# Performance work log

Hardware: AMD Instinct MI355X
Metric: run time of the kernel (lower is better)

The kernel has to match this reference:

```python
import jax, jax.numpy as jnp
import numpy as np

EPS = 1e-6
ALPHA = 0.2  # LeakyReLU negative slope


def layer_norm(x, g, b):
    mu = jnp.mean(x, axis=-1, keepdims=True)
    var = jnp.mean(jnp.square(x - mu), axis=-1, keepdims=True)
    return (x - mu) * jax.lax.rsqrt(var + EPS) * g + b


def graph_attention(x, bias, W, a_src, a_dst):
    # x: [B,N,D], bias: [B,N,N], W: [D, H*Dh], a_src/a_dst: [H, Dh]
    B, N, D = x.shape
    H, Dh = a_src.shape
    h = jnp.einsum('bnd,dhk->bhnk', x, W.reshape(D, H, Dh))  # [B,H,N,Dh]
    s = jnp.einsum('bhnk,hk->bhn', h, a_src)                 # source term
    t = jnp.einsum('bhnk,hk->bhn', h, a_dst)                 # target term
    e = jax.nn.leaky_relu(s[:, :, :, None] + t[:, :, None, :], ALPHA)
    e = e + bias[:, None, :, :]                              # graph mask/bias
    attn = jax.nn.softmax(e, axis=-1)                        # [B,H,N,N]
    out = jnp.einsum('bhij,bhjk->bhik', attn, h)             # [B,H,N,Dh]
    return out.transpose(0, 2, 1, 3).reshape(B, N, H * Dh)


def setup_inputs() -> dict:
    key = jax.random.key(0)
    ks = jax.random.split(key, 8)
    B, N, D, H = 2, 2048, 512, 8
    Dh = D // H
    sc = 1.0 / np.sqrt(D)
    return {
        'x': jax.random.normal(ks[0], (B, N, D), jnp.float32),
        'bias': jax.random.normal(ks[1], (B, N, N), jnp.float32),
        'W1': jax.random.normal(ks[2], (D, D), jnp.float32) * sc,
        'a_src1': jax.random.normal(ks[3], (H, Dh), jnp.float32) * sc,
        'a_dst1': jax.random.normal(ks[4], (H, Dh), jnp.float32) * sc,
        'g1': jnp.ones((D,), jnp.float32),
        'b1': jnp.zeros((D,), jnp.float32),
        'W2': jax.random.normal(ks[5], (D, D), jnp.float32) * sc,
        'a_src2': jax.random.normal(ks[6], (1, D), jnp.float32) * sc,
        'a_dst2': jax.random.normal(ks[7], (1, D), jnp.float32) * sc,
        'g2': jnp.ones((D,), jnp.float32),
        'b2': jnp.zeros((D,), jnp.float32),
    }


def reference(x, bias, W1, a_src1, a_dst1, g1, b1, W2, a_src2, a_dst2, g2, b2):
    # dropout is identity in eval mode
    attn_in = layer_norm(x, g1, b1)
    attn = graph_attention(attn_in, bias, W1, a_src1, a_dst1) + x
    attn_in2 = layer_norm(attn, g2, b2)
    out = graph_attention(attn_in2, bias, W2, a_src2, a_dst2) + attn
    return out
```

## Files before the change

kernel.cpp:

```cpp
#include <hip/hip_runtime.h>
#include <math.h>

#define NB 2
#define NN 2048
#define DD 512
#define L2E 1.44269504088896340736f

typedef __attribute__((ext_vector_type(8))) short short8;
typedef __attribute__((ext_vector_type(4))) float f32x4;

__device__ __forceinline__ unsigned short f2bf(float x) {
  union { float f; unsigned u; } a;
  a.f = x;
  unsigned r = a.u + 0x7FFF + ((a.u >> 16) & 1);
  return (unsigned short)(r >> 16);
}
__device__ __forceinline__ float bf2f(unsigned short u) {
  union { unsigned u; float f; } a;
  a.u = ((unsigned)u) << 16;
  return a.f;
}
__device__ __forceinline__ unsigned cvtpk(float lo, float hi) {
  unsigned r;
  asm("v_cvt_pk_bf16_f32 %0, %1, %2" : "=v"(r) : "v"(lo), "v"(hi));
  return r;
}
__device__ __forceinline__ uint2 exp4pk(float e0, float e1, float e2, float e3) {
  float p0, p1, p2, p3;
  uint2 d;
  asm("v_exp_f32 %2, %6\n\t"
      "v_exp_f32 %3, %7\n\t"
      "v_exp_f32 %4, %8\n\t"
      "v_exp_f32 %5, %9\n\t"
      "v_cvt_pk_bf16_f32 %0, %2, %3\n\t"
      "v_cvt_pk_bf16_f32 %1, %4, %5"
      : "=&v"(d.x), "=&v"(d.y), "=&v"(p0), "=&v"(p1), "=&v"(p2), "=&v"(p3)
      : "v"(e0), "v"(e1), "v"(e2), "v"(e3));
  return d;
}

__device__ __forceinline__ float waveReduceSum(float v) {
#pragma unroll
  for (int o = 32; o; o >>= 1) v += __shfl_down(v, o, 64);
  return v;
}
__device__ __forceinline__ float blockReduceSum(float v, float* red4) {
  int tid = threadIdx.x;
  __syncthreads();
  v = waveReduceSum(v);
  if ((tid & 63) == 0) red4[tid >> 6] = v;
  __syncthreads();
  return red4[0] + red4[1] + red4[2] + red4[3];
}

__global__ __launch_bounds__(256) void prep_kernel(
    const float* __restrict__ W1, const float* __restrict__ W2,
    unsigned short* __restrict__ WT1, unsigned short* __restrict__ WT2,
    const float* __restrict__ as1, const float* __restrict__ ad1,
    float* __restrict__ vs1, float* __restrict__ vd1,
    const float* __restrict__ as2, const float* __restrict__ ad2,
    float* __restrict__ vs2, float* __restrict__ vd2) {
  __shared__ float tile[64][65];
  int bid = blockIdx.x;
  int t = threadIdx.x;
  if (bid < 128) {
    const float* W = (bid & 64) ? W2 : W1;
    unsigned short* WT = (bid & 64) ? WT2 : WT1;
    int r = bid & 63;
    int kt = (r >> 3) * 64, ct = (r & 7) * 64;
#pragma unroll
    for (int u = 0; u < 16; u++) {
      int lin = t + u * 256;
      int kl = lin >> 6, cl = lin & 63;
      tile[kl][cl] = W[(size_t)(kt + kl) * DD + ct + cl];
    }
    __syncthreads();
#pragma unroll
    for (int u = 0; u < 16; u++) {
      int lin = t + u * 256;
      int cl = lin >> 6, kl = lin & 63;
      WT[(size_t)(ct + cl) * DD + kt + kl] = f2bf(tile[kl][cl]);
    }
  } else {
    int idx = bid - 128;
    int slot = idx >> 3, dch = idx & 7;
    const float *W, *as, *ad;
    float *vs, *vd;
    int Dh, hoff;
    if (slot < 8) {
      W = W1; as = as1 + slot * 64; ad = ad1 + slot * 64;
      vs = vs1 + (size_t)slot * DD; vd = vd1 + (size_t)slot * DD;
      Dh = 64; hoff = slot * 64;
    } else {
      W = W2; as = as2; ad = ad2; vs = vs2; vd = vd2;
      Dh = 512; hoff = 0;
    }
    int dl = t >> 2, kq = t & 3;
    int d = dch * 64 + dl;
    int kn = Dh >> 2;
    const float* wr = W + (size_t)d * DD + hoff + kq * kn;
    const float* asp = as + kq * kn;
    const float* adp = ad + kq * kn;
    float s = 0.f, dd2 = 0.f;
    for (int k = 0; k < kn; k++) {
      float wv = wr[k];
      s += wv * asp[k];
      dd2 += wv * adp[k];
    }
    s += __shfl_xor(s, 1);
    s += __shfl_xor(s, 2);
    dd2 += __shfl_xor(dd2, 1);
    dd2 += __shfl_xor(dd2, 2);
    if (kq == 0) {
      vs[d] = s;
      vd[d] = dd2;
    }
  }
}

__global__ __launch_bounds__(256) void lnst_kernel(
    const float* __restrict__ x, const float* __restrict__ g,
    const float* __restrict__ bb, unsigned short* __restrict__ y,
    const float* __restrict__ vs, const float* __restrict__ vd,
    float* __restrict__ sOut, float* __restrict__ tOut, int HN) {
  __shared__ float red4[4];
  __shared__ float lnS[512];
  int row = blockIdx.x;
  int t = threadIdx.x;
  const float* xr = x + (size_t)row * DD;
  float2 v = *(const float2*)&xr[2 * t];
  float s = blockReduceSum(v.x + v.y, red4);
  float mu = s * (1.0f / 512.0f);
  float d0 = v.x - mu, d1 = v.y - mu;
  float ss = blockReduceSum(d0 * d0 + d1 * d1, red4);
  float rstd = rsqrtf(ss * (1.0f / 512.0f) + 1e-6f);
  float2 gg = *(const float2*)&g[2 * t];
  float2 bv = *(const float2*)&bb[2 * t];
  float n0 = d0 * rstd * gg.x + bv.x;
  float n1 = d1 * rstd * gg.y + bv.y;
  ushort2 o;
  o.x = f2bf(n0);
  o.y = f2bf(n1);
  *(ushort2*)&y[(size_t)row * DD + 2 * t] = o;
  lnS[2 * t] = n0;
  lnS[2 * t + 1] = n1;
  __syncthreads();
  int wv = t >> 6, l = t & 63;
  int b = row >> 11, n = row & (NN - 1);
  float4 x0 = *(const float4*)&lnS[l * 8];
  float4 x1 = *(const float4*)&lnS[l * 8 + 4];
  for (int h = wv; h < HN; h += 4) {
    const float* vsr = vs + (size_t)h * DD + l * 8;
    const float* vdr = vd + (size_t)h * DD + l * 8;
    float4 a0 = *(const float4*)vsr, a1 = *(const float4*)(vsr + 4);
    float4 c0 = *(const float4*)vdr, c1 = *(const float4*)(vdr + 4);
    float ps = x0.x * a0.x + x0.y * a0.y + x0.z * a0.z + x0.w * a0.w +
               x1.x * a1.x + x1.y * a1.y + x1.z * a1.z + x1.w * a1.w;
    float pd = x0.x * c0.x + x0.y * c0.y + x0.z * c0.z + x0.w * c0.w +
               x1.x * c1.x + x1.y * c1.y + x1.z * c1.z + x1.w * c1.w;
#pragma unroll
    for (int o2 = 32; o2; o2 >>= 1) {
      ps += __shfl_xor(ps, o2);
      pd += __shfl_xor(pd, o2);
    }
    if (l == 0) {
      sOut[((size_t)b * HN + h) * NN + n] = ps * L2E;
      tOut[((size_t)b * HN + h) * NN + n] = pd * L2E;
    }
  }
}

__global__ __launch_bounds__(256) void gemm_kernel(const unsigned short* __restrict__ A,
                                                   const unsigned short* __restrict__ BT,
                                                   unsigned short* __restrict__ hbT) {
  __shared__ float accL[4][16][65];
  int t = threadIdx.x, w = t >> 6, l = t & 63;
  int li = l & 15, lg = l >> 4;
  int R0 = blockIdx.x * 16;
  int c0 = blockIdx.y * 64;
  const unsigned short* ar = A + (size_t)(R0 + li) * DD + w * 128 + lg * 8;
  const unsigned short* br = BT + (size_t)(c0 + li) * DD + w * 128 + lg * 8;
  f32x4 acc[4] = {};
#pragma unroll
  for (int k0 = 0; k0 < 128; k0 += 32) {
    short8 af = *(const short8*)(ar + k0);
#pragma unroll
    for (int f = 0; f < 4; f++) {
      short8 bf = *(const short8*)(br + (size_t)f * 16 * DD + k0);
      acc[f] = __builtin_amdgcn_mfma_f32_16x16x32_bf16(af, bf, acc[f], 0, 0, 0);
    }
  }
#pragma unroll
  for (int f = 0; f < 4; f++)
#pragma unroll
    for (int r = 0; r < 4; r++) accL[w][lg * 4 + r][f * 16 + li] = acc[f][r];
  __syncthreads();
  int b = R0 >> 11, jT = (R0 & (NN - 1)) >> 4;
#pragma unroll
  for (int u = 0; u < 2; u++) {
    int idx = t + u * 256;
    int f = idx >> 7;
    int rem = idx & 127;
    int cl = rem >> 3, jlp = rem & 7;
    int cc = f * 16 + cl;
    float v0 = accL[0][2 * jlp][cc] + accL[1][2 * jlp][cc] + accL[2][2 * jlp][cc] +
               accL[3][2 * jlp][cc];
    float v1 = accL[0][2 * jlp + 1][cc] + accL[1][2 * jlp + 1][cc] +
               accL[2][2 * jlp + 1][cc] + accL[3][2 * jlp + 1][cc];
    size_t off = (((size_t)(b * (DD / 64) + blockIdx.y) * (NN / 16)) + jT) * 1024 +
                 f * 256 + cl * 16 + jlp * 2;
    *(unsigned*)(hbT + off) = cvtpk(v0, v1);
  }
}

template <int HN, int CCH>
__global__ __launch_bounds__(256) void pv_kernel(
    const unsigned short* __restrict__ hbT, const float* __restrict__ bias,
    const float* __restrict__ sArr, const float* __restrict__ tArr,
    const float* __restrict__ res, float* __restrict__ out) {
  constexpr int DH = DD / HN;
  __shared__ __align__(16) unsigned char smem[16640];
  unsigned short (*Pl)[2][1024] = (unsigned short (*)[2][1024])smem;
  float (*accL)[16][33] = (float (*)[16][33])smem;
  float (*sLa)[16] = (float (*)[16])(smem + 8448);
  int t = threadIdx.x, w = t >> 6, l = t & 63;
  int li = l & 15, lg = l >> 4;
  int i0 = blockIdx.x * 16;
  int ck = blockIdx.y, bh = blockIdx.z;
  int h = bh % HN, b = bh / HN;
  int c0 = h * DH + ck * (CCH * 64);
  size_t bhN = (size_t)bh * NN;
  const float* trow = tArr + bhN;

  int rs = l >> 3, js = (l & 7) * 8, jc = l & 7;
  int wchunk = ((jc & 4) | ((jc & 3) ^ (rs & 3))) * 8;
  float sv[2];
  sv[0] = sArr[bhN + i0 + rs];
  sv[1] = sArr[bhN + i0 + 8 + rs];
  const float* bb0 = bias + ((size_t)b * NN + i0 + rs) * NN;
  const float* bb1 = bb0 + (size_t)8 * NN;

  const unsigned short* vbase =
      hbT + ((size_t)(b * (DD / 64) + (c0 >> 6)) * (NN / 16)) * 1024 +
      (lg >> 1) * 1024 + li * 16 + (lg & 1) * 8;
  int ra0 = li * 64 + (lg ^ (li & 3)) * 8;
  int ra1 = ra0 + 32;

  union { short8 v; unsigned short q[8]; } ones;
#pragma unroll
  for (int k = 0; k < 8; k++) ones.q[k] = 0x3F80;

  const int jbeg = w * (NN / 4), jend = jbeg + NN / 4;
  f32x4 acc[CCH][4] = {};
  f32x4 accS = {0.f, 0.f, 0.f, 0.f};

  auto loadTB = [&](int j, float4& t0, float4& t1, float4& b0a, float4& b0b,
                    float4& b1a, float4& b1b) {
    t0 = *(const float4*)&trow[j + js];
    t1 = *(const float4*)&trow[j + js + 4];
    b0a = *(const float4*)&bb0[j + js];
    b0b = *(const float4*)&bb0[j + js + 4];
    b1a = *(const float4*)&bb1[j + js];
    b1b = *(const float4*)&bb1[j + js + 4];
  };
  auto computeP = [&](const float4& t0, const float4& t1, const float4& b0a,
                      const float4& b0b, const float4& b1a, const float4& b1b, int pb) {
#pragma unroll
    for (int u = 0; u < 2; u++) {
      const float4& ba = u ? b1a : b0a;
      const float4& bc = u ? b1b : b0b;
      int row = u * 8 + rs;
      float e0 = sv[u] + t0.x, e1 = sv[u] + t0.y;
      float e2 = sv[u] + t0.z, e3 = sv[u] + t0.w;
      float e4 = sv[u] + t1.x, e5 = sv[u] + t1.y;
      float e6 = sv[u] + t1.z, e7 = sv[u] + t1.w;
      e0 = fmaf(ba.x, L2E, fmaxf(e0, 0.2f * e0));
      e1 = fmaf(ba.y, L2E, fmaxf(e1, 0.2f * e1));
      e2 = fmaf(ba.z, L2E, fmaxf(e2, 0.2f * e2));
      e3 = fmaf(ba.w, L2E, fmaxf(e3, 0.2f * e3));
      e4 = fmaf(bc.x, L2E, fmaxf(e4, 0.2f * e4));
      e5 = fmaf(bc.y, L2E, fmaxf(e5, 0.2f * e5));
      e6 = fmaf(bc.z, L2E, fmaxf(e6, 0.2f * e6));
      e7 = fmaf(bc.w, L2E, fmaxf(e7, 0.2f * e7));
      uint2 d0 = exp4pk(e0, e1, e2, e3);
      uint2 d1 = exp4pk(e4, e5, e6, e7);
      uint4 dd;
      dd.x = d0.x; dd.y = d0.y; dd.z = d1.x; dd.w = d1.y;
      *(uint4*)&Pl[w][pb][row * 64 + wchunk] = dd;
    }
  };
  auto loadV = [&](int jt, short8 (&vv)[CCH][8]) {
#pragma unroll
    for (int cc = 0; cc < CCH; cc++) {
      const unsigned short* vp =
          vbase + (size_t)cc * ((NN / 16) * 1024) + (size_t)jt * 64;
#pragma unroll
      for (int f = 0; f < 4; f++) {
        vv[cc][f] = *(const short8*)(vp + f * 256);
        vv[cc][4 + f] = *(const short8*)(vp + 2048 + f * 256);
      }
    }
  };
  auto domfma = [&](short8 a0, short8 a1, const short8 (&vv)[CCH][8]) {
    __builtin_amdgcn_s_setprio(1);
    accS = __builtin_amdgcn_mfma_f32_16x16x32_bf16(a0, ones.v, accS, 0, 0, 0);
#pragma unroll
    for (int cc = 0; cc < CCH; cc++)
#pragma unroll
      for (int f = 0; f < 4; f++)
        acc[cc][f] =
            __builtin_amdgcn_mfma_f32_16x16x32_bf16(a0, vv[cc][f], acc[cc][f], 0, 0, 0);
    accS = __builtin_amdgcn_mfma_f32_16x16x32_bf16(a1, ones.v, accS, 0, 0, 0);
#pragma unroll
    for (int cc = 0; cc < CCH; cc++)
#pragma unroll
      for (int f = 0; f < 4; f++)
        acc[cc][f] =
            __builtin_amdgcn_mfma_f32_16x16x32_bf16(a1, vv[cc][4 + f], acc[cc][f], 0, 0, 0);
    __builtin_amdgcn_s_setprio(0);
  };

  float4 tA0, tA1, bA0, bA1, bA2, bA3;
  short8 vv[CCH][8];

  loadTB(jbeg, tA0, tA1, bA0, bA1, bA2, bA3);
  computeP(tA0, tA1, bA0, bA1, bA2, bA3, 0);
  loadTB(jbeg + 64, tA0, tA1, bA0, bA1, bA2, bA3);

  int buf = 0;
  for (int jt = jbeg; jt < jend; jt += 64) {
    loadV(jt, vv);
    short8 a0 = *(const short8*)&Pl[w][buf][ra0];
    short8 a1 = *(const short8*)&Pl[w][buf][ra1];
    if (jt + 64 < jend) {
      float4 n0 = tA0, n1 = tA1, m0 = bA0, m1 = bA1, m2 = bA2, m3 = bA3;
      int jn = (jt + 128 < jend) ? (jt + 128) : jbeg;
      loadTB(jn, tA0, tA1, bA0, bA1, bA2, bA3);
      computeP(n0, n1, m0, m1, m2, m3, buf ^ 1);
    }
    domfma(a0, a1, vv);
    buf ^= 1;
  }

  __syncthreads();
  if (li == 0) {
#pragma unroll
    for (int r = 0; r < 4; r++) sLa[w][lg * 4 + r] = accS[r];
  }
#pragma unroll
  for (int g = 0; g < 2 * CCH; g++) {
    int cc = g >> 1, half = g & 1;
#pragma unroll
    for (int f = 0; f < 2; f++)
#pragma unroll
      for (int r = 0; r < 4; r++)
        accL[w][lg * 4 + r][f * 16 + li] = acc[cc][half * 2 + f][r];
    __syncthreads();
    {
      int rr = t >> 4, cp = (t & 15) * 2;
      float S = sLa[0][rr] + sLa[1][rr] + sLa[2][rr] + sLa[3][rr];
      float inv = 1.0f / S;
      float2 O = {0.f, 0.f};
#pragma unroll
      for (int w2 = 0; w2 < 4; w2++) {
        O.x += accL[w2][rr][cp];
        O.y += accL[w2][rr][cp + 1];
      }
      size_t ix = ((size_t)b * NN + i0 + rr) * DD + c0 + cc * 64 + half * 32 + cp;
      float2 rv = *(const float2*)&res[ix];
      float2 ov = {O.x * inv + rv.x, O.y * inv + rv.y};
      *(float2*)&out[ix] = ov;
    }
    __syncthreads();
  }
}

extern "C" void kernel_launch(void* const* d_in, const int* in_sizes, int n_in,
                              void* d_out, int out_size, void* d_ws, size_t ws_size,
                              hipStream_t stream) {
  const float* x = (const float*)d_in[0];
  const float* bias = (const float*)d_in[1];
  const float* W1 = (const float*)d_in[2];
  const float* asrc1 = (const float*)d_in[3];
  const float* adst1 = (const float*)d_in[4];
  const float* g1 = (const float*)d_in[5];
  const float* b1 = (const float*)d_in[6];
  const float* W2 = (const float*)d_in[7];
  const float* asrc2 = (const float*)d_in[8];
  const float* adst2 = (const float*)d_in[9];
  const float* g2 = (const float*)d_in[10];
  const float* b2 = (const float*)d_in[11];
  float* out = (float*)d_out;
  float* ws = (float*)d_ws;

  const size_t RC = (size_t)NB * NN * DD;
  float* attnBuf = ws;
  unsigned short* lnB = (unsigned short*)(ws + RC);
  unsigned short* hbT = (unsigned short*)(ws + RC + RC / 2);
  unsigned short* WT1 = (unsigned short*)(ws + 2 * RC);
  unsigned short* WT2 = WT1 + (size_t)DD * DD;
  float* vs1 = (float*)(WT2 + (size_t)DD * DD);
  float* vd1 = vs1 + 8 * DD;
  float* vs2 = vd1 + 8 * DD;
  float* vd2 = vs2 + DD;
  float* sBuf = vd2 + DD;
  float* tBuf = sBuf + 16 * NN;

  const int rows = NB * NN;

  hipLaunchKernelGGL(prep_kernel, dim3(128 + 72), dim3(256), 0, stream, W1, W2, WT1, WT2,
                     asrc1, adst1, vs1, vd1, asrc2, adst2, vs2, vd2);

  hipLaunchKernelGGL(lnst_kernel, dim3(rows), dim3(256), 0, stream, x, g1, b1, lnB, vs1, vd1,
                     sBuf, tBuf, 8);
  hipLaunchKernelGGL(gemm_kernel, dim3(256, 8), dim3(256), 0, stream, lnB, WT1, hbT);
  hipLaunchKernelGGL((pv_kernel<8, 1>), dim3(128, 1, 16), dim3(256), 0, stream, hbT, bias,
                     sBuf, tBuf, x, attnBuf);

  hipLaunchKernelGGL(lnst_kernel, dim3(rows), dim3(256), 0, stream, attnBuf, g2, b2, lnB, vs2,
                     vd2, sBuf, tBuf, 1);
  hipLaunchKernelGGL(gemm_kernel, dim3(256, 8), dim3(256), 0, stream, lnB, WT2, hbT);
  hipLaunchKernelGGL((pv_kernel<1, 2>), dim3(128, 4, 2), dim3(256), 0, stream, hbT, bias,
                     sBuf, tBuf, attnBuf, out);
}
```

Measured before the change: 153.1 us.

## Split PV work across two column groups per block with double-buffered V loads

Replaces pv_kernel with pvg_kernel, in which each block handles two 64-column groups. Pairs of waves split the key range in halves instead of four waves splitting it in quarters. The main loop is unrolled by two so V fragments for the next tile load into a second register set while the current MFMAs run. The epilogue reduces across two waves per group instead of four. Layer 1 now uses the same grid shape as layer 2. The aim is better latency hiding and less cross-wave reduction, at the cost of more registers and recomputing P per column group in layer 2.

New measurement: 160.1 us. 4.6% more time.

```diff
diff --git a/kernel.cpp b/kernel.cpp
--- a/kernel.cpp
+++ b/kernel.cpp
@@ -213,23 +213,22 @@
   }
 }
 
-template <int HN, int CCH>
-__global__ __launch_bounds__(256) void pv_kernel(
+template <int HN>
+__global__ __launch_bounds__(256) void pvg_kernel(
     const unsigned short* __restrict__ hbT, const float* __restrict__ bias,
     const float* __restrict__ sArr, const float* __restrict__ tArr,
     const float* __restrict__ res, float* __restrict__ out) {
-  constexpr int DH = DD / HN;
-  __shared__ __align__(16) unsigned char smem[16640];
+  __shared__ __align__(16) unsigned char smem[16896];
   unsigned short (*Pl)[2][1024] = (unsigned short (*)[2][1024])smem;
-  float (*accL)[16][33] = (float (*)[16][33])smem;
-  float (*sLa)[16] = (float (*)[16])(smem + 8448);
+  float (*accL2)[16][65] = (float (*)[16][65])smem;
+  float (*sLa)[16] = (float (*)[16])(smem + 8320);
   int t = threadIdx.x, w = t >> 6, l = t & 63;
+  int jh = w & 1, hp = w >> 1;
   int li = l & 15, lg = l >> 4;
   int i0 = blockIdx.x * 16;
-  int ck = blockIdx.y, bh = blockIdx.z;
-  int h = bh % HN, b = bh / HN;
-  int c0 = h * DH + ck * (CCH * 64);
-  size_t bhN = (size_t)bh * NN;
+  int g0 = blockIdx.y * 2, b = blockIdx.z;
+  int grp = g0 + hp;
+  size_t bhN = ((size_t)b * HN + (HN == 8 ? grp : 0)) * NN;
   const float* trow = tArr + bhN;
 
   int rs = l >> 3, js = (l & 7) * 8, jc = l & 7;
@@ -241,8 +240,8 @@
   const float* bb1 = bb0 + (size_t)8 * NN;
 
   const unsigned short* vbase =
-      hbT + ((size_t)(b * (DD / 64) + (c0 >> 6)) * (NN / 16)) * 1024 +
-      (lg >> 1) * 1024 + li * 16 + (lg & 1) * 8;
+      hbT + ((size_t)(b * 8 + grp) * (NN / 16)) * 1024 + (lg >> 1) * 1024 + li * 16 +
+      (lg & 1) * 8;
   int ra0 = li * 64 + (lg ^ (li & 3)) * 8;
   int ra1 = ra0 + 32;
 
@@ -250,8 +249,8 @@
 #pragma unroll
   for (int k = 0; k < 8; k++) ones.q[k] = 0x3F80;
 
-  const int jbeg = w * (NN / 4), jend = jbeg + NN / 4;
-  f32x4 acc[CCH][4] = {};
+  const int jbeg = jh * (NN / 2), jend = jbeg + NN / 2;
+  f32x4 acc[4] = {};
   f32x4 accS = {0.f, 0.f, 0.f, 0.f};
 
   auto loadTB = [&](int j, float4& t0, float4& t1, float4& b0a, float4& b0b,
@@ -289,57 +288,59 @@
       *(uint4*)&Pl[w][pb][row * 64 + wchunk] = dd;
     }
   };
-  auto loadV = [&](int jt, short8 (&vv)[CCH][8]) {
-#pragma unroll
-    for (int cc = 0; cc < CCH; cc++) {
-      const unsigned short* vp =
-          vbase + (size_t)cc * ((NN / 16) * 1024) + (size_t)jt * 64;
-#pragma unroll
-      for (int f = 0; f < 4; f++) {
-        vv[cc][f] = *(const short8*)(vp + f * 256);
-        vv[cc][4 + f] = *(const short8*)(vp + 2048 + f * 256);
-      }
+  auto loadV = [&](int jt, short8 (&vv)[8]) {
+    const unsigned short* vp = vbase + (size_t)jt * 64;
+#pragma unroll
+    for (int f = 0; f < 4; f++) {
+      vv[f] = *(const short8*)(vp + f * 256);
+      vv[4 + f] = *(const short8*)(vp + 2048 + f * 256);
     }
   };
-  auto domfma = [&](short8 a0, short8 a1, const short8 (&vv)[CCH][8]) {
+  auto domfma = [&](short8 a0, short8 a1, const short8 (&vv)[8]) {
     __builtin_amdgcn_s_setprio(1);
     accS = __builtin_amdgcn_mfma_f32_16x16x32_bf16(a0, ones.v, accS, 0, 0, 0);
-#pragma unroll
-    for (int cc = 0; cc < CCH; cc++)
-#pragma unroll
-      for (int f = 0; f < 4; f++)
-        acc[cc][f] =
-            __builtin_amdgcn_mfma_f32_16x16x32_bf16(a0, vv[cc][f], acc[cc][f], 0, 0, 0);
+    acc[0] = __builtin_amdgcn_mfma_f32_16x16x32_bf16(a0, vv[0], acc[0], 0, 0, 0);
+    acc[1] = __builtin_amdgcn_mfma_f32_16x16x32_bf16(a0, vv[1], acc[1], 0, 0, 0);
+    acc[2] = __builtin_amdgcn_mfma_f32_16x16x32_bf16(a0, vv[2], acc[2], 0, 0, 0);
+    acc[3] = __builtin_amdgcn_mfma_f32_16x16x32_bf16(a0, vv[3], acc[3], 0, 0, 0);
     accS = __builtin_amdgcn_mfma_f32_16x16x32_bf16(a1, ones.v, accS, 0, 0, 0);
-#pragma unroll
-    for (int cc = 0; cc < CCH; cc++)
-#pragma unroll
-      for (int f = 0; f < 4; f++)
-        acc[cc][f] =
-            __builtin_amdgcn_mfma_f32_16x16x32_bf16(a1, vv[cc][4 + f], acc[cc][f], 0, 0, 0);
+    acc[0] = __builtin_amdgcn_mfma_f32_16x16x32_bf16(a1, vv[4], acc[0], 0, 0, 0);
+    acc[1] = __builtin_amdgcn_mfma_f32_16x16x32_bf16(a1, vv[5], acc[1], 0, 0, 0);
+    acc[2] = __builtin_amdgcn_mfma_f32_16x16x32_bf16(a1, vv[6], acc[2], 0, 0, 0);
+    acc[3] = __builtin_amdgcn_mfma_f32_16x16x32_bf16(a1, vv[7], acc[3], 0, 0, 0);
     __builtin_amdgcn_s_setprio(0);
   };
 
   float4 tA0, tA1, bA0, bA1, bA2, bA3;
-  short8 vv[CCH][8];
+  short8 vvA[8], vvB[8];
 
   loadTB(jbeg, tA0, tA1, bA0, bA1, bA2, bA3);
   computeP(tA0, tA1, bA0, bA1, bA2, bA3, 0);
   loadTB(jbeg + 64, tA0, tA1, bA0, bA1, bA2, bA3);
-
-  int buf = 0;
-  for (int jt = jbeg; jt < jend; jt += 64) {
-    loadV(jt, vv);
-    short8 a0 = *(const short8*)&Pl[w][buf][ra0];
-    short8 a1 = *(const short8*)&Pl[w][buf][ra1];
-    if (jt + 64 < jend) {
+  loadV(jbeg, vvA);
+
+  for (int jt = jbeg; jt < jend; jt += 128) {
+    loadV(jt + 64, vvB);
+    short8 a0 = *(const short8*)&Pl[w][0][ra0];
+    short8 a1 = *(const short8*)&Pl[w][0][ra1];
+    {
       float4 n0 = tA0, n1 = tA1, m0 = bA0, m1 = bA1, m2 = bA2, m3 = bA3;
       int jn = (jt + 128 < jend) ? (jt + 128) : jbeg;
       loadTB(jn, tA0, tA1, bA0, bA1, bA2, bA3);
-      computeP(n0, n1, m0, m1, m2, m3, buf ^ 1);
-    }
-    domfma(a0, a1, vv);
-    buf ^= 1;
+      computeP(n0, n1, m0, m1, m2, m3, 1);
+    }
+    domfma(a0, a1, vvA);
+    bool more = (jt + 128 < jend);
+    if (more) loadV(jt + 128, vvA);
+    short8 c0 = *(const short8*)&Pl[w][1][ra0];
+    short8 c1 = *(const short8*)&Pl[w][1][ra1];
+    if (more) {
+      float4 n0 = tA0, n1 = tA1, m0 = bA0, m1 = bA1, m2 = bA2, m3 = bA3;
+      int jn = (jt + 192 < jend) ? (jt + 192) : jbeg;
+      loadTB(jn, tA0, tA1, bA0, bA1, bA2, bA3);
+      computeP(n0, n1, m0, m1, m2, m3, 0);
+    }
+    domfma(c0, c1, vvB);
   }
 
   __syncthreads();
@@ -348,28 +349,25 @@
     for (int r = 0; r < 4; r++) sLa[w][lg * 4 + r] = accS[r];
   }
 #pragma unroll
-  for (int g = 0; g < 2 * CCH; g++) {
-    int cc = g >> 1, half = g & 1;
-#pragma unroll
-    for (int f = 0; f < 2; f++)
-#pragma unroll
-      for (int r = 0; r < 4; r++)
-        accL[w][lg * 4 + r][f * 16 + li] = acc[cc][half * 2 + f][r];
+  for (int hp2 = 0; hp2 < 2; hp2++) {
+    if (hp == hp2) {
+#pragma unroll
+      for (int f = 0; f < 4; f++)
+#pragma unroll
+        for (int r = 0; r < 4; r++) accL2[jh][lg * 4 + r][f * 16 + li] = acc[f][r];
+    }
     __syncthreads();
     {
-      int rr = t >> 4, cp = (t & 15) * 2;
-      float S = sLa[0][rr] + sLa[1][rr] + sLa[2][rr] + sLa[3][rr];
+      int rr = t >> 4, cq = t & 15;
+      float S = sLa[2 * hp2][rr] + sLa[2 * hp2 + 1][rr];
       float inv = 1.0f / S;
-      float2 O = {0.f, 0.f};
-#pragma unroll
-      for (int w2 = 0; w2 < 4; w2++) {
-        O.x += accL[w2][rr][cp];
-        O.y += accL[w2][rr][cp + 1];
+      size_t ixb = ((size_t)b * NN + i0 + rr) * DD + (g0 + hp2) * 64 + cq;
+#pragma unroll
+      for (int f = 0; f < 4; f++) {
+        int col = f * 16 + cq;
+        float O = accL2[0][rr][col] + accL2[1][rr][col];
+        out[ixb + f * 16] = O * inv + res[ixb + f * 16];
       }
-      size_t ix = ((size_t)b * NN + i0 + rr) * DD + c0 + cc * 64 + half * 32 + cp;
-      float2 rv = *(const float2*)&res[ix];
-      float2 ov = {O.x * inv + rv.x, O.y * inv + rv.y};
-      *(float2*)&out[ix] = ov;
     }
     __syncthreads();
   }
@@ -414,12 +412,12 @@
   hipLaunchKernelGGL(lnst_kernel, dim3(rows), dim3(256), 0, stream, x, g1, b1, lnB, vs1, vd1,
                      sBuf, tBuf, 8);
   hipLaunchKernelGGL(gemm_kernel, dim3(256, 8), dim3(256), 0, stream, lnB, WT1, hbT);
-  hipLaunchKernelGGL((pv_kernel<8, 1>), dim3(128, 1, 16), dim3(256), 0, stream, hbT, bias,
-                     sBuf, tBuf, x, attnBuf);
+  hipLaunchKernelGGL(pvg_kernel<8>, dim3(128, 4, 2), dim3(256), 0, stream, hbT, bias, sBuf,
+                     tBuf, x, attnBuf);
 
   hipLaunchKernelGGL(lnst_kernel, dim3(rows), dim3(256), 0, stream, attnBuf, g2, b2, lnB, vs2,
                      vd2, sBuf, tBuf, 1);
   hipLaunchKernelGGL(gemm_kernel, dim3(256, 8), dim3(256), 0, stream, lnB, WT2, hbT);
-  hipLaunchKernelGGL((pv_kernel<1, 2>), dim3(128, 4, 2), dim3(256), 0, stream, hbT, bias,
-                     sBuf, tBuf, attnBuf, out);
-}
+  hipLaunchKernelGGL(pvg_kernel<1>, dim3(128, 4, 2), dim3(256), 0, stream, hbT, bias, sBuf,
+                     tBuf, attnBuf, out);
+}
```
